# Performance work log

Measured on AMD Instinct MI355X. Metric: run time of the kernel, lower is better.

Reference implementation:

```python
import jax, jax.numpy as jnp
import numpy as np

HID = 2048; NH = 16; NKV = 2; HD = 128; G = NH // NKV
SEC = (16, 24, 24)  # sums to 64 = HD/2
EPS = 1e-6
B, S = 2, 1024


def _reorder(table):
    # table: [3, B, S, HD]; interleave sections picking axis i%3 per chunk
    chunks = []
    idx = 0
    for _ in range(2):
        for sec in SEC:
            chunks.append(table[..., idx:idx + sec])
            idx += sec
    return jnp.concatenate([c[i % len(SEC)] for i, c in enumerate(chunks)], axis=-1)  # [B,S,HD]


def rotate_half(x):
    x1, x2 = jnp.split(x, 2, axis=-1)
    return jnp.concatenate((-x2, x1), axis=-1)


def rms_norm(x, gamma):
    var = jnp.mean(jnp.square(x), axis=-1, keepdims=True)
    return gamma * (x * jax.lax.rsqrt(var + EPS))


def setup_inputs() -> dict:
    key = jax.random.key(0)
    ks = jax.random.split(key, 12)
    x = jax.random.normal(ks[0], (B, S, HID), dtype=jnp.float32)
    ang = jax.random.uniform(ks[1], (3, B, S, HD), dtype=jnp.float32) * 6.28318
    cos = jnp.cos(ang)
    sin = jnp.sin(ang)
    mask = jnp.ones((B, S), dtype=jnp.float32)
    sc = 0.02
    q_w = jax.random.normal(ks[2], (HID, NH * HD), dtype=jnp.float32) * sc
    q_b = jnp.zeros((NH * HD,), dtype=jnp.float32)
    k_w = jax.random.normal(ks[3], (HID, NKV * HD), dtype=jnp.float32) * sc
    k_b = jnp.zeros((NKV * HD,), dtype=jnp.float32)
    v_w = jax.random.normal(ks[4], (HID, NKV * HD), dtype=jnp.float32) * sc
    v_b = jnp.zeros((NKV * HD,), dtype=jnp.float32)
    q_gamma = jnp.ones((HD,), dtype=jnp.float32)
    k_gamma = jnp.ones((HD,), dtype=jnp.float32)
    o_w = jax.random.normal(ks[5], (NH * HD, HID), dtype=jnp.float32) * sc
    return {"x": x, "cos": cos, "sin": sin, "mask": mask,
            "q_w": q_w, "q_b": q_b, "k_w": k_w, "k_b": k_b,
            "v_w": v_w, "v_b": v_b, "q_gamma": q_gamma, "k_gamma": k_gamma,
            "o_w": o_w}


def reference(x, cos, sin, mask, q_w, q_b, k_w, k_b, v_w, v_b, q_gamma, k_gamma, o_w):
    b, s, _ = x.shape
    # QKV projections
    q = (x @ q_w + q_b).reshape(b, s, NH, HD)
    k = (x @ k_w + k_b).reshape(b, s, NKV, HD)
    v = (x @ v_w + v_b).reshape(b, s, NKV, HD)
    # per-head RMSNorm on q, k
    q = rms_norm(q, q_gamma)
    k = rms_norm(k, k_gamma)
    q = jnp.transpose(q, (0, 2, 1, 3))  # [B,NH,S,HD]
    k = jnp.transpose(k, (0, 2, 1, 3))  # [B,NKV,S,HD]
    v = jnp.transpose(v, (0, 2, 1, 3))
    # multimodal RoPE
    cos_f = _reorder(cos)[:, None, :, :]  # [B,1,S,HD]
    sin_f = _reorder(sin)[:, None, :, :]
    q = q * cos_f + rotate_half(q) * sin_f
    k = k * cos_f + rotate_half(k) * sin_f
    # key-mask zeroing and effective lengths
    eff = mask.sum(axis=-1).astype(jnp.int32)  # [B]
    bm = mask[:, None, :, None]
    k = k * bm
    v = v * bm
    hist = (jnp.arange(s)[None, :] < eff[:, None]).astype(jnp.float32)  # [B,S]
    # GQA attention scores in fp32
    qg = q.reshape(b, NKV, G, s, HD)
    scores = jnp.einsum('bngqd,bnkd->bngqk', qg, k,
                        precision=jax.lax.Precision.HIGHEST) * (HD ** -0.5)
    scores = scores.reshape(b, NH, s, s)
    scores = scores + (1.0 - hist)[:, None, None, :] * -1e9
    causal = jnp.tril(jnp.ones((s, s), dtype=jnp.float32))
    scores = scores + (1.0 - causal)[None, None, :, :] * -1e9
    aw = jax.nn.softmax(scores, axis=-1)
    # weighted values
    out = jnp.einsum('bngqk,bnkd->bngqd', aw.reshape(b, NKV, G, s, s), v,
                     precision=jax.lax.Precision.HIGHEST)
    out = out.reshape(b, NH, s, HD)
    out = jnp.transpose(out, (0, 2, 1, 3)).reshape(b, s, NH * HD)
    return out @ o_w
```

## Files before the change

### kernel.cpp

```cpp
#include <hip/hip_runtime.h>

typedef __attribute__((ext_vector_type(8))) short bf16x8;
typedef __attribute__((ext_vector_type(4))) float f32x4;

#define MFMA16(a, b, c) __builtin_amdgcn_mfma_f32_16x16x32_bf16(a, b, c, 0, 0, 0)

__device__ inline short f2bf(float f) {
  union { float f; unsigned u; } v;
  v.f = f;
  unsigned r = v.u + 0x7FFF + ((v.u >> 16) & 1);
  return (short)(r >> 16);
}
__device__ inline float bf2f(short s) {
  union { unsigned u; float f; } v;
  v.u = ((unsigned)(unsigned short)s) << 16;
  return v.f;
}
#define GLD_LDS16(g, l)                                                        \
  __builtin_amdgcn_global_load_lds(                                            \
      (const __attribute__((address_space(1))) unsigned int*)(g),              \
      (__attribute__((address_space(3))) unsigned int*)(l), 16, 0, 0)

__device__ __forceinline__ void raw_barrier() {
  __asm__ volatile("" ::: "memory");
  __builtin_amdgcn_s_barrier();
  __asm__ volatile("" ::: "memory");
}

__global__ __launch_bounds__(256) void prep_kernel(
    const float* __restrict__ x, const float* __restrict__ q_w,
    const float* __restrict__ k_w, const float* __restrict__ v_w,
    const float* __restrict__ o_w, short* __restrict__ xb,
    short* __restrict__ wqkv_t, short* __restrict__ wo_t) {
  __shared__ float t[64][65];
  int bid = blockIdx.x;
  if (bid < 4096) {
    int i = (bid * 256 + threadIdx.x) * 4;
    float4 f = *(const float4*)&x[i];
    short4 o;
    o.x = f2bf(f.x); o.y = f2bf(f.y); o.z = f2bf(f.z); o.w = f2bf(f.w);
    *(short4*)&xb[i] = o;
    return;
  }
  bid -= 4096;
  const float* src;
  short* dst;
  int C, bx, by;
  if (bid < 1024) {
    src = q_w; dst = wqkv_t; C = 2048;
    bx = (bid & 31) * 64; by = (bid >> 5) * 64;
  } else if (bid < 1152) {
    bid -= 1024;
    src = k_w; dst = wqkv_t + (size_t)2048 * 2048; C = 256;
    bx = (bid & 3) * 64; by = (bid >> 2) * 64;
  } else if (bid < 1280) {
    bid -= 1152;
    src = v_w; dst = wqkv_t + (size_t)2304 * 2048; C = 256;
    bx = (bid & 3) * 64; by = (bid >> 2) * 64;
  } else {
    bid -= 1280;
    src = o_w; dst = wo_t; C = 2048;
    bx = (bid & 31) * 64; by = (bid >> 5) * 64;
  }
  const int R = 2048;
  const int tx = threadIdx.x & 15;
  const int ty = threadIdx.x >> 4;
#pragma unroll
  for (int i = 0; i < 4; i++) {
    int row = ty + i * 16;
    float4 f = *(const float4*)&src[(size_t)(by + row) * C + bx + tx * 4];
    t[row][tx * 4 + 0] = f.x;
    t[row][tx * 4 + 1] = f.y;
    t[row][tx * 4 + 2] = f.z;
    t[row][tx * 4 + 3] = f.w;
  }
  __syncthreads();
#pragma unroll
  for (int i = 0; i < 4; i++) {
    int c = ty + i * 16;
    short4 o;
    o.x = f2bf(t[tx * 4 + 0][c]);
    o.y = f2bf(t[tx * 4 + 1][c]);
    o.z = f2bf(t[tx * 4 + 2][c]);
    o.w = f2bf(t[tx * 4 + 3][c]);
    *(short4*)&dst[(size_t)(bx + c) * R + by + tx * 4] = o;
  }
}

__global__ __launch_bounds__(256) void gemm_db_kernel(const short* __restrict__ A,
                                                      const short* __restrict__ B,
                                                      float* __restrict__ C, int N,
                                                      int gx, int gy) {
  __shared__ __align__(16) short As[4][64 * 32];
  __shared__ __align__(16) short Bs[4][128 * 32];
  const int bid = blockIdx.x;
  const int xcd = bid & 7, idx = bid >> 3;
  const int colsPerX = gx >> 1, rowsPerX = gy >> 2;
  const int xt = (xcd & 1) * colsPerX + idx % colsPerX;
  const int yt = (xcd >> 1) * rowsPerX + idx / colsPerX;
  const int tid = threadIdx.x;
  const int lane = tid & 63, wave = tid >> 6;
  const int quad = lane >> 4, l16 = lane & 15;
  const int m0 = yt * 64, n0 = xt * 128;
  const int wm = (wave >> 1) * 32, wn = (wave & 1) * 64;
  const int r0 = tid >> 2, c0 = (tid & 3) * 8;
  const int ca = c0 ^ ((r0 & 3) << 3);
  const size_t arow = (size_t)(m0 + r0) * 2048;
  const size_t brow0 = (size_t)(n0 + r0) * 2048, brow1 = (size_t)(n0 + r0 + 64) * 2048;
  f32x4 acc[2][4];
#pragma unroll
  for (int mi = 0; mi < 2; mi++)
#pragma unroll
    for (int ni = 0; ni < 4; ni++) acc[mi][ni] = (f32x4){0.f, 0.f, 0.f, 0.f};

#pragma unroll
  for (int st = 0; st < 4; st++) {
    const int kk = st * 32 + ca;
    GLD_LDS16(&A[arow + kk], &As[st][r0 * 32 + c0]);
    GLD_LDS16(&B[brow0 + kk], &Bs[st][r0 * 32 + c0]);
    GLD_LDS16(&B[brow1 + kk], &Bs[st][(r0 + 64) * 32 + c0]);
  }

  const int sx = (l16 & 3) << 3;
  for (int p = 0; p < 32; p++) {
    if (p < 31) {
      __asm__ volatile("s_waitcnt vmcnt(6)" ::: "memory");
    } else {
      __asm__ volatile("s_waitcnt vmcnt(0)" ::: "memory");
    }
    raw_barrier();
#pragma unroll
    for (int j = 0; j < 2; j++) {
      const int cur = (2 * p + j) & 3;
      bf16x8 af[2], bfr[4];
#pragma unroll
      for (int mi = 0; mi < 2; mi++)
        af[mi] = *(const bf16x8*)&As[cur][(wm + mi * 16 + l16) * 32 + ((quad * 8) ^ sx)];
#pragma unroll
      for (int ni = 0; ni < 4; ni++)
        bfr[ni] = *(const bf16x8*)&Bs[cur][(wn + ni * 16 + l16) * 32 + ((quad * 8) ^ sx)];
#pragma unroll
      for (int mi = 0; mi < 2; mi++)
#pragma unroll
        for (int ni = 0; ni < 4; ni++)
          acc[mi][ni] = MFMA16(af[mi], bfr[ni], acc[mi][ni]);
    }
    __asm__ volatile("s_waitcnt lgkmcnt(0)" ::: "memory");
    raw_barrier();
    if (p < 30) {
#pragma unroll
      for (int j = 0; j < 2; j++) {
        const int st = 2 * p + 4 + j;
        const int slot = st & 3;
        const int kk = st * 32 + ca;
        GLD_LDS16(&A[arow + kk], &As[slot][r0 * 32 + c0]);
        GLD_LDS16(&B[brow0 + kk], &Bs[slot][r0 * 32 + c0]);
        GLD_LDS16(&B[brow1 + kk], &Bs[slot][(r0 + 64) * 32 + c0]);
      }
    }
  }
#pragma unroll
  for (int mi = 0; mi < 2; mi++)
#pragma unroll
    for (int ni = 0; ni < 4; ni++)
#pragma unroll
      for (int r = 0; r < 4; r++)
        C[(size_t)(m0 + wm + mi * 16 + quad * 4 + r) * N + n0 + wn + ni * 16 + l16] =
            acc[mi][ni][r];
}

__global__ __launch_bounds__(256) void postv_kernel(
    const float* __restrict__ qkv, const float* __restrict__ qbias,
    const float* __restrict__ kbias, const float* __restrict__ vbias,
    const float* __restrict__ qg, const float* __restrict__ kg,
    const float* __restrict__ cosb, const float* __restrict__ sinb,
    const float* __restrict__ maskp, short* __restrict__ qo, short* __restrict__ ko,
    short* __restrict__ vtb) {
  __shared__ short t[32][33];
  const int bid = blockIdx.x;
  if (bid < 9216) {
    const int rid = bid * 4 + (threadIdx.x >> 6);
    const int lane = threadIdx.x & 63;
    const int slot = rid >> 11;
    const int bs = rid & 2047;
    const int b = bs >> 10, s = bs & 1023;
    const float* row = qkv + (size_t)bs * 2560;
    int off;
    const float* bias;
    const float* gamma;
    if (slot < 16) { off = slot * 128; bias = qbias + slot * 128; gamma = qg; }
    else { off = 2048 + (slot - 16) * 128; bias = kbias + (slot - 16) * 128; gamma = kg; }
    float v0 = row[off + lane] + bias[lane];
    float v1 = row[off + 64 + lane] + bias[64 + lane];
    float ss = v0 * v0 + v1 * v1;
#pragma unroll
    for (int o = 1; o < 64; o <<= 1) ss += __shfl_xor(ss, o);
    float r = rsqrtf(ss * (1.0f / 128.0f) + 1e-6f);
    v0 = gamma[lane] * v0 * r;
    v1 = gamma[64 + lane] * v1 * r;
    int sel = (lane < 16) ? 0 : (lane < 40) ? 1 : 2;
    size_t ci = ((size_t)(sel * 2 + b) * 1024 + s) * 128 + lane;
    float c0 = cosb[ci], s0 = sinb[ci], c1 = cosb[ci + 64], s1 = sinb[ci + 64];
    float o0 = v0 * c0 - v1 * s0;
    float o1 = v1 * c1 + v0 * s1;
    if (slot >= 16) { float mk = maskp[bs]; o0 *= mk; o1 *= mk; }
    size_t oidx;
    short* optr;
    if (slot < 16) { oidx = (((size_t)(b * 16 + slot) * 1024) + s) * 128; optr = qo; }
    else { oidx = (((size_t)(b * 2 + (slot - 16)) * 1024) + s) * 128; optr = ko; }
    optr[oidx + lane] = f2bf(o0);
    optr[oidx + 64 + lane] = f2bf(o1);
    return;
  }
  const int b2 = bid - 9216;
  const int d0 = (b2 & 3) * 32;
  const int s0 = ((b2 >> 2) & 31) * 32;
  const int bz = b2 >> 7;
  const int bq = bz >> 1, kv = bz & 1;
  const int tx = threadIdx.x & 31;
  const int ty = threadIdx.x >> 5;
#pragma unroll
  for (int i = 0; i < 4; i++) {
    int s = s0 + ty + i * 8;
    float val = qkv[((size_t)(bq * 1024 + s)) * 2560 + 2304 + kv * 128 + d0 + tx] +
                vbias[kv * 128 + d0 + tx];
    t[ty + i * 8][tx] = f2bf(val * maskp[bq * 1024 + s]);
  }
  __syncthreads();
#pragma unroll
  for (int i = 0; i < 4; i++)
    vtb[((size_t)bz * 128 + d0 + ty + i * 8) * 1024 + s0 + tx] = t[tx][ty + i * 8];
}

__global__ __launch_bounds__(256) void attn_kernel(const short* __restrict__ Q,
                                                   const short* __restrict__ K,
                                                   const short* __restrict__ Vt_g,
                                                   short* __restrict__ po,
                                                   float* __restrict__ pml) {
  int x = blockIdx.x;
  const int h = blockIdx.y;
  const int b = blockIdx.z;
  int g = 0, base = 0;
  while (x >= base + 4 * (g + 1)) { base += 4 * (g + 1); g++; }
  const int r0 = x - base;
  const int qt = 4 * g + r0 / (g + 1);
  const int kc = r0 % (g + 1);
  int nsteps = qt - 4 * kc + 1;
  if (nsteps > 4) nsteps = 4;

  const int kv = h >> 3;
  const int tid = threadIdx.x;
  const int wave = tid >> 6, lane = tid & 63;
  const int quad = lane >> 4, l16 = lane & 15;
  __shared__ __align__(16) short Ks[64 * 136];
  __shared__ __align__(16) short Vs[128 * 72];
  __shared__ __align__(16) short Ps[4][16 * 68];

  const size_t qoff = (((size_t)(b * 16 + h) * 1024) + qt * 64 + wave * 16 + l16) * 128;
  bf16x8 aq[4];
#pragma unroll
  for (int kk = 0; kk < 4; kk++) aq[kk] = *(const bf16x8*)&Q[qoff + kk * 32 + quad * 8];

  f32x4 o[8];
#pragma unroll
  for (int i = 0; i < 8; i++) o[i] = (f32x4){0.f, 0.f, 0.f, 0.f};
  float l[4] = {0.f, 0.f, 0.f, 0.f};
  const int qrow0 = qt * 64 + wave * 16 + quad * 4;
  const size_t koff = ((size_t)(b * 2 + kv) * 1024) * 128;
  const size_t voff = koff;
  const float scale = 0.08838834764831845f;

  for (int st = 0; st < nsteps; st++) {
    const int ks0 = kc * 256 + st * 64;
#pragma unroll
    for (int it = 0; it < 4; it++) {
      int c = it * 256 + tid;
      {
        int row = c >> 4, cc = (c & 15) * 8;
        *(int4*)&Ks[row * 136 + cc] =
            *(const int4*)&K[koff + (size_t)(ks0 + row) * 128 + cc];
      }
      {
        int d = c >> 3, cc = (c & 7) * 8;
        *(int4*)&Vs[d * 72 + cc] =
            *(const int4*)&Vt_g[voff + (size_t)d * 1024 + ks0 + cc];
      }
    }
    __syncthreads();
    f32x4 sc[4];
#pragma unroll
    for (int nt = 0; nt < 4; nt++) sc[nt] = (f32x4){0.f, 0.f, 0.f, 0.f};
#pragma unroll
    for (int nt = 0; nt < 4; nt++)
#pragma unroll
      for (int kk = 0; kk < 4; kk++) {
        bf16x8 bk = *(const bf16x8*)&Ks[(nt * 16 + l16) * 136 + kk * 32 + quad * 8];
        sc[nt] = MFMA16(aq[kk], bk, sc[nt]);
      }
    short* P = &Ps[wave][0];
#pragma unroll
    for (int nt = 0; nt < 4; nt++) {
      const int kcol = ks0 + nt * 16 + l16;
#pragma unroll
      for (int r = 0; r < 4; r++) {
        float p = (kcol > qrow0 + r) ? 0.f : __expf(fmaf(sc[nt][r], scale, -12.0f));
        l[r] += p;
        P[(quad * 4 + r) * 68 + nt * 16 + l16] = f2bf(p);
      }
    }
    __asm__ volatile("s_waitcnt lgkmcnt(0)" ::: "memory");
    bf16x8 pa0 = *(const bf16x8*)&P[l16 * 68 + quad * 8];
    bf16x8 pa1 = *(const bf16x8*)&P[l16 * 68 + 32 + quad * 8];
#pragma unroll
    for (int nt = 0; nt < 8; nt++) {
      bf16x8 bv0 = *(const bf16x8*)&Vs[(nt * 16 + l16) * 72 + quad * 8];
      bf16x8 bv1 = *(const bf16x8*)&Vs[(nt * 16 + l16) * 72 + 32 + quad * 8];
      o[nt] = MFMA16(pa0, bv0, o[nt]);
      o[nt] = MFMA16(pa1, bv1, o[nt]);
    }
    __syncthreads();
  }
#pragma unroll
  for (int off = 1; off < 16; off <<= 1)
#pragma unroll
    for (int r = 0; r < 4; r++) l[r] += __shfl_xor(l[r], off);
  const int p = (b * 16 + h) * 40 + blockIdx.x;
  const int lrow = wave * 16 + quad * 4;
#pragma unroll
  for (int nt = 0; nt < 8; nt++)
#pragma unroll
    for (int r = 0; r < 4; r++)
      po[(size_t)p * 8192 + (size_t)(lrow + r) * 128 + nt * 16 + l16] = f2bf(o[nt][r]);
  if (l16 == 0) {
#pragma unroll
    for (int r = 0; r < 4; r++) pml[(size_t)p * 64 + lrow + r] = l[r];
  }
}

__global__ __launch_bounds__(256) void attn_combine_kernel(const short* __restrict__ po,
                                                           const float* __restrict__ pml,
                                                           short* __restrict__ attn) {
  const int qt = blockIdx.x, h = blockIdx.y, b = blockIdx.z;
  const int g = qt >> 2, nc = g + 1;
  const int x0 = 2 * g * (g + 1) + (qt & 3) * nc;
  const int row = threadIdx.x >> 2;
  const int d0 = (threadIdx.x & 3) * 32;
  const int pbase = (b * 16 + h) * 40 + x0;
  float denom = 0.f;
#pragma unroll
  for (int kc = 0; kc < 4; kc++)
    if (kc < nc) denom += pml[(size_t)(pbase + kc) * 64 + row];
  float inv = 1.f / denom;
  float acc[32];
#pragma unroll
  for (int j = 0; j < 32; j++) acc[j] = 0.f;
#pragma unroll
  for (int kc = 0; kc < 4; kc++)
    if (kc < nc) {
      const short* src = po + (size_t)(pbase + kc) * 8192 + (size_t)row * 128 + d0;
#pragma unroll
      for (int j = 0; j < 4; j++) {
        int4 v = *(const int4*)&src[j * 8];
        const short* vs = (const short*)&v;
#pragma unroll
        for (int e = 0; e < 8; e++) acc[j * 8 + e] += bf2f(vs[e]);
      }
    }
  short ob[32];
#pragma unroll
  for (int j = 0; j < 32; j++) ob[j] = f2bf(acc[j] * inv);
  short* dst = attn + ((size_t)(b * 1024 + qt * 64 + row)) * 2048 + h * 128 + d0;
#pragma unroll
  for (int j = 0; j < 4; j++) *(int4*)&dst[j * 8] = *(const int4*)&ob[j * 8];
}

extern "C" void kernel_launch(void* const* d_in, const int* in_sizes, int n_in,
                              void* d_out, int out_size, void* d_ws, size_t ws_size,
                              hipStream_t stream) {
  const float* x = (const float*)d_in[0];
  const float* cosb = (const float*)d_in[1];
  const float* sinb = (const float*)d_in[2];
  const float* mask = (const float*)d_in[3];
  const float* q_w = (const float*)d_in[4];
  const float* q_b = (const float*)d_in[5];
  const float* k_w = (const float*)d_in[6];
  const float* k_b = (const float*)d_in[7];
  const float* v_w = (const float*)d_in[8];
  const float* v_b = (const float*)d_in[9];
  const float* qg = (const float*)d_in[10];
  const float* kg = (const float*)d_in[11];
  const float* o_w = (const float*)d_in[12];
  float* out = (float*)d_out;

  char* ws = (char*)d_ws;
  short* wo_t = (short*)(ws);
  short* wqkv_t = (short*)(ws + ((size_t)8 << 20));
  float* pml = (float*)(ws + ((size_t)8 << 20));
  short* attn = (short*)(ws + ((size_t)9 << 20));
  short* xb = (short*)(ws + ((size_t)18 << 20));
  short* qb = xb;
  float* qkv_raw = (float*)(ws + ((size_t)26 << 20));
  short* po = (short*)(ws + ((size_t)26 << 20));
  short* kb = (short*)(ws + ((size_t)46 << 20));
  short* vtb = (short*)(ws + ((size_t)47 << 20));

  prep_kernel<<<6400, 256, 0, stream>>>(x, q_w, k_w, v_w, o_w, xb, wqkv_t, wo_t);
  gemm_db_kernel<<<640, 256, 0, stream>>>(xb, wqkv_t, qkv_raw, 2560, 20, 32);
  postv_kernel<<<9728, 256, 0, stream>>>(qkv_raw, q_b, k_b, v_b, qg, kg, cosb, sinb, mask,
                                         qb, kb, vtb);
  attn_kernel<<<dim3(40, 16, 2), 256, 0, stream>>>(qb, kb, vtb, po, pml);
  attn_combine_kernel<<<dim3(16, 16, 2), 256, 0, stream>>>(po, pml, attn);
  gemm_db_kernel<<<512, 256, 0, stream>>>(attn, wo_t, out, 2048, 16, 32);
}
```

Measured before the change: 233.3 us.

## Prefetch next K/V tile into registers and XOR-swizzle LDS layout

The attention partial kernel now loads the next K and V tiles from global memory into registers while the current tile's MFMA work runs. The register-staged data is written to LDS at the start of the next step. The padded LDS layouts for K and V are replaced by unpadded rows with an XOR swizzle of 16-byte slots, which avoids bank conflicts and shrinks LDS usage. The P scratch stride changes from 68 to 72. This adds register pressure from the eight int4 prefetch buffers, which may reduce occupancy.

```diff
diff --git a/kernel.cpp b/kernel.cpp
--- a/kernel.cpp
+++ b/kernel.cpp
@@ -252,9 +252,9 @@
   const int tid = threadIdx.x;
   const int wave = tid >> 6, lane = tid & 63;
   const int quad = lane >> 4, l16 = lane & 15;
-  __shared__ __align__(16) short Ks[64 * 136];
-  __shared__ __align__(16) short Vs[128 * 72];
-  __shared__ __align__(16) short Ps[4][16 * 68];
+  __shared__ __align__(16) short Ks[64 * 128];
+  __shared__ __align__(16) short Vs[128 * 64];
+  __shared__ __align__(16) short Ps[4][16 * 72];
 
   const size_t qoff = (((size_t)(b * 16 + h) * 1024) + qt * 64 + wave * 16 + l16) * 128;
   bf16x8 aq[4];
@@ -270,33 +270,54 @@
   const size_t voff = koff;
   const float scale = 0.08838834764831845f;
 
+  int4 kreg[4], vreg[4];
+  {
+    const int ks0 = kc * 256;
+#pragma unroll
+    for (int it = 0; it < 4; it++) {
+      int c = it * 256 + tid;
+      kreg[it] = *(const int4*)&K[koff + (size_t)(ks0 + (c >> 4)) * 128 + (c & 15) * 8];
+      vreg[it] = *(const int4*)&Vt_g[voff + (size_t)(c >> 3) * 1024 + ks0 + (c & 7) * 8];
+    }
+  }
+
   for (int st = 0; st < nsteps; st++) {
-    const int ks0 = kc * 256 + st * 64;
+    __syncthreads();
 #pragma unroll
     for (int it = 0; it < 4; it++) {
       int c = it * 256 + tid;
       {
-        int row = c >> 4, cc = (c & 15) * 8;
-        *(int4*)&Ks[row * 136 + cc] =
-            *(const int4*)&K[koff + (size_t)(ks0 + row) * 128 + cc];
+        int row = c >> 4, sl = c & 15;
+        *(int4*)&Ks[row * 128 + ((sl ^ (row & 7)) * 8)] = kreg[it];
       }
       {
-        int d = c >> 3, cc = (c & 7) * 8;
-        *(int4*)&Vs[d * 72 + cc] =
-            *(const int4*)&Vt_g[voff + (size_t)d * 1024 + ks0 + cc];
+        int d = c >> 3, sl = c & 7;
+        *(int4*)&Vs[d * 64 + ((sl ^ (d & 7)) * 8)] = vreg[it];
       }
     }
     __syncthreads();
+    if (st + 1 < nsteps) {
+      const int ksn = kc * 256 + (st + 1) * 64;
+#pragma unroll
+      for (int it = 0; it < 4; it++) {
+        int c = it * 256 + tid;
+        kreg[it] = *(const int4*)&K[koff + (size_t)(ksn + (c >> 4)) * 128 + (c & 15) * 8];
+        vreg[it] = *(const int4*)&Vt_g[voff + (size_t)(c >> 3) * 1024 + ksn + (c & 7) * 8];
+      }
+    }
+    const int ks0 = kc * 256 + st * 64;
     f32x4 sc[4];
 #pragma unroll
     for (int nt = 0; nt < 4; nt++) sc[nt] = (f32x4){0.f, 0.f, 0.f, 0.f};
 #pragma unroll
-    for (int nt = 0; nt < 4; nt++)
+    for (int nt = 0; nt < 4; nt++) {
+      const int rr = nt * 16 + l16;
 #pragma unroll
       for (int kk = 0; kk < 4; kk++) {
-        bf16x8 bk = *(const bf16x8*)&Ks[(nt * 16 + l16) * 136 + kk * 32 + quad * 8];
+        bf16x8 bk = *(const bf16x8*)&Ks[rr * 128 + (((kk * 4 + quad) ^ (rr & 7)) * 8)];
         sc[nt] = MFMA16(aq[kk], bk, sc[nt]);
       }
+    }
     short* P = &Ps[wave][0];
 #pragma unroll
     for (int nt = 0; nt < 4; nt++) {
@@ -305,20 +326,20 @@
       for (int r = 0; r < 4; r++) {
         float p = (kcol > qrow0 + r) ? 0.f : __expf(fmaf(sc[nt][r], scale, -12.0f));
         l[r] += p;
-        P[(quad * 4 + r) * 68 + nt * 16 + l16] = f2bf(p);
+        P[(quad * 4 + r) * 72 + nt * 16 + l16] = f2bf(p);
       }
     }
     __asm__ volatile("s_waitcnt lgkmcnt(0)" ::: "memory");
-    bf16x8 pa0 = *(const bf16x8*)&P[l16 * 68 + quad * 8];
-    bf16x8 pa1 = *(const bf16x8*)&P[l16 * 68 + 32 + quad * 8];
+    bf16x8 pa0 = *(const bf16x8*)&P[l16 * 72 + quad * 8];
+    bf16x8 pa1 = *(const bf16x8*)&P[l16 * 72 + 32 + quad * 8];
 #pragma unroll
     for (int nt = 0; nt < 8; nt++) {
-      bf16x8 bv0 = *(const bf16x8*)&Vs[(nt * 16 + l16) * 72 + quad * 8];
-      bf16x8 bv1 = *(const bf16x8*)&Vs[(nt * 16 + l16) * 72 + 32 + quad * 8];
+      const int rr = nt * 16 + l16;
+      bf16x8 bv0 = *(const bf16x8*)&Vs[rr * 64 + ((quad ^ (rr & 7)) * 8)];
+      bf16x8 bv1 = *(const bf16x8*)&Vs[rr * 64 + (((4 + quad) ^ (rr & 7)) * 8)];
       o[nt] = MFMA16(pa0, bv0, o[nt]);
       o[nt] = MFMA16(pa1, bv1, o[nt]);
     }
-    __syncthreads();
   }
 #pragma unroll
   for (int off = 1; off < 16; off <<= 1)
```

New measurement: 258.5 us. 10.8% more time.

## Double-buffer K/V tiles via async global-to-LDS loads with XOR swizzle

Applied to the files above, without the earlier changes.

The attention partial kernel now stages K and V tiles directly from global memory into LDS using global_load_lds, into two buffers, so the next tile's load overlaps the current tile's MFMA work. Padded LDS rows are replaced by an XOR swizzle of 16-byte chunks to avoid bank conflicts, and the P scratch pitch changes from 68 to 72. The per-step barrier at the loop end is removed and replaced by a vmcnt wait plus a raw barrier at the loop start. This relies on the single barrier being enough to keep a buffer from being overwritten while other waves still read it.

```diff
diff --git a/kernel.cpp b/kernel.cpp
--- a/kernel.cpp
+++ b/kernel.cpp
@@ -252,9 +252,9 @@
   const int tid = threadIdx.x;
   const int wave = tid >> 6, lane = tid & 63;
   const int quad = lane >> 4, l16 = lane & 15;
-  __shared__ __align__(16) short Ks[64 * 136];
-  __shared__ __align__(16) short Vs[128 * 72];
-  __shared__ __align__(16) short Ps[4][16 * 68];
+  __shared__ __align__(16) short Ks[2][64 * 128];
+  __shared__ __align__(16) short Vs[2][128 * 64];
+  __shared__ __align__(16) short Ps[4][16 * 72];
 
   const size_t qoff = (((size_t)(b * 16 + h) * 1024) + qt * 64 + wave * 16 + l16) * 128;
   bf16x8 aq[4];
@@ -270,33 +270,39 @@
   const size_t voff = koff;
   const float scale = 0.08838834764831845f;
 
+#define STAGE_KV(bf, ks0)                                                          \
+  {                                                                                \
+    _Pragma("unroll") for (int it = 0; it < 4; it++) {                             \
+      const int c = it * 256 + tid;                                                \
+      const int row = c >> 4, sl = c & 15;                                         \
+      GLD_LDS16(&K[koff + (size_t)((ks0) + row) * 128 + ((sl ^ (row & 7)) * 8)],   \
+                &Ks[bf][c * 8]);                                                   \
+      const int d = c >> 3, sv = c & 7;                                            \
+      GLD_LDS16(&Vt_g[voff + (size_t)d * 1024 + (ks0) + ((sv ^ (d & 7)) * 8)],     \
+                &Vs[bf][c * 8]);                                                   \
+    }                                                                              \
+  }
+
+  STAGE_KV(0, kc * 256);
+
   for (int st = 0; st < nsteps; st++) {
+    __asm__ volatile("s_waitcnt vmcnt(0)" ::: "memory");
+    raw_barrier();
+    if (st + 1 < nsteps) { STAGE_KV((st + 1) & 1, kc * 256 + (st + 1) * 64); }
+    const int cb = st & 1;
     const int ks0 = kc * 256 + st * 64;
-#pragma unroll
-    for (int it = 0; it < 4; it++) {
-      int c = it * 256 + tid;
-      {
-        int row = c >> 4, cc = (c & 15) * 8;
-        *(int4*)&Ks[row * 136 + cc] =
-            *(const int4*)&K[koff + (size_t)(ks0 + row) * 128 + cc];
-      }
-      {
-        int d = c >> 3, cc = (c & 7) * 8;
-        *(int4*)&Vs[d * 72 + cc] =
-            *(const int4*)&Vt_g[voff + (size_t)d * 1024 + ks0 + cc];
-      }
-    }
-    __syncthreads();
     f32x4 sc[4];
 #pragma unroll
     for (int nt = 0; nt < 4; nt++) sc[nt] = (f32x4){0.f, 0.f, 0.f, 0.f};
 #pragma unroll
-    for (int nt = 0; nt < 4; nt++)
+    for (int nt = 0; nt < 4; nt++) {
+      const int rr = nt * 16 + l16;
 #pragma unroll
       for (int kk = 0; kk < 4; kk++) {
-        bf16x8 bk = *(const bf16x8*)&Ks[(nt * 16 + l16) * 136 + kk * 32 + quad * 8];
+        bf16x8 bk = *(const bf16x8*)&Ks[cb][rr * 128 + (((kk * 4 + quad) ^ (rr & 7)) * 8)];
         sc[nt] = MFMA16(aq[kk], bk, sc[nt]);
       }
+    }
     short* P = &Ps[wave][0];
 #pragma unroll
     for (int nt = 0; nt < 4; nt++) {
@@ -305,21 +311,22 @@
       for (int r = 0; r < 4; r++) {
         float p = (kcol > qrow0 + r) ? 0.f : __expf(fmaf(sc[nt][r], scale, -12.0f));
         l[r] += p;
-        P[(quad * 4 + r) * 68 + nt * 16 + l16] = f2bf(p);
+        P[(quad * 4 + r) * 72 + nt * 16 + l16] = f2bf(p);
       }
     }
     __asm__ volatile("s_waitcnt lgkmcnt(0)" ::: "memory");
-    bf16x8 pa0 = *(const bf16x8*)&P[l16 * 68 + quad * 8];
-    bf16x8 pa1 = *(const bf16x8*)&P[l16 * 68 + 32 + quad * 8];
+    bf16x8 pa0 = *(const bf16x8*)&P[l16 * 72 + quad * 8];
+    bf16x8 pa1 = *(const bf16x8*)&P[l16 * 72 + 32 + quad * 8];
 #pragma unroll
     for (int nt = 0; nt < 8; nt++) {
-      bf16x8 bv0 = *(const bf16x8*)&Vs[(nt * 16 + l16) * 72 + quad * 8];
-      bf16x8 bv1 = *(const bf16x8*)&Vs[(nt * 16 + l16) * 72 + 32 + quad * 8];
+      const int rr = nt * 16 + l16;
+      bf16x8 bv0 = *(const bf16x8*)&Vs[cb][rr * 64 + ((quad ^ (rr & 7)) * 8)];
+      bf16x8 bv1 = *(const bf16x8*)&Vs[cb][rr * 64 + (((4 + quad) ^ (rr & 7)) * 8)];
       o[nt] = MFMA16(pa0, bv0, o[nt]);
       o[nt] = MFMA16(pa1, bv1, o[nt]);
     }
-    __syncthreads();
-  }
+  }
+#undef STAGE_KV
 #pragma unroll
   for (int off = 1; off < 16; off <<= 1)
 #pragma unroll
```

After: 223.9 us. 1.04x faster.
